# Kernel optimization log

Hardware: AMD Instinct MI355X
Metric: run time of the kernel (lower is better)

Reference implementation:

```python
import jax, jax.numpy as jnp
import numpy as np

B, N, K = 4, 100000, 128
Q_MIN = 0.5
S_B = 1.0
POT_SCALE = 1.0
REP_SCALE = 1.0
BETA_SCALE = 1.0
E_WEIGHT = 1.0
POS_WEIGHT = 1.0
TIME_WEIGHT = 1.0
HUBER_D = 2.0


def setup_inputs() -> dict:
    key = jax.random.key(0)
    ks = jax.random.split(key, 9)
    return {
        "beta": jax.random.uniform(ks[0], (B, N), dtype=jnp.float32),
        "ccoords": jax.random.normal(ks[1], (B, N, 2), dtype=jnp.float32),
        "pred_energy": jax.random.uniform(ks[2], (B, N), dtype=jnp.float32),
        "pred_pos": jax.random.normal(ks[3], (B, N, 2), dtype=jnp.float32),
        "pred_time": jax.random.uniform(ks[4], (B, N), dtype=jnp.float32),
        "t_energy": jax.random.uniform(ks[5], (B, N), dtype=jnp.float32),
        "t_pos": jax.random.normal(ks[6], (B, N, 2), dtype=jnp.float32),
        "t_time": jax.random.uniform(ks[7], (B, N), dtype=jnp.float32),
        "t_idx": jax.random.randint(ks[8], (B, N), 0, K + 1, dtype=jnp.int32),
    }


def _huber(x, d):
    a = jnp.abs(x)
    return jnp.where(a <= d, 0.5 * x * x, d * (a - 0.5 * d))


def _oc_loss(beta, ccoords, pred_energy, pred_pos, pred_time,
             t_energy, t_pos, t_time, t_idx):
    eps = 1e-4
    beta = jnp.clip(beta, eps, 1.0 - eps)
    q = jnp.arctanh(beta) ** 2 + Q_MIN                     # [B,N]

    obj = t_idx - 1                                        # -1 = noise, 0..K-1 = object id
    M = obj[:, :, None] == jnp.arange(K, dtype=jnp.int32)  # [B,N,K] bool membership
    Mf = M.astype(q.dtype)
    obj_exists = jnp.any(M, axis=1)                        # [B,K]
    exf = obj_exists.astype(q.dtype)

    # condensation point per object = member hit with max charge q (segment argmax)
    q_masked = jnp.where(M, q[:, :, None], -1.0)           # [B,N,K]
    alpha = jnp.argmax(q_masked, axis=1)                   # [B,K]
    x_alpha = jnp.take_along_axis(ccoords, alpha[:, :, None], axis=1)  # [B,K,2]
    q_alpha = jnp.take_along_axis(q, alpha, axis=1)        # [B,K]
    beta_alpha = jnp.take_along_axis(beta, alpha, axis=1)  # [B,K]

    # pairwise hit <-> condensation-point distances, [B,N,K]
    diff = ccoords[:, :, None, :] - x_alpha[:, None, :, :]
    dist = jnp.sqrt(jnp.sum(diff * diff, axis=-1) + 1e-12)

    qq = q[:, :, None] * q_alpha[:, None, :] * exf[:, None, :]
    v_att = qq * (dist * dist) * Mf
    v_rep = qq * jax.nn.relu(1.0 - dist) * (1.0 - Mf)
    n_tot = jnp.asarray(B * N, q.dtype)
    L_att = jnp.sum(v_att) / n_tot
    L_rep = jnp.sum(v_rep) / n_tot

    # beta loss: pull condensation-point betas to 1, suppress noise betas
    n_obj = jnp.maximum(jnp.sum(exf), 1.0)
    L_beta_obj = jnp.sum((1.0 - beta_alpha) * exf) / n_obj
    noise = (t_idx == 0).astype(q.dtype)
    L_noise = jnp.sum(beta * noise) / jnp.maximum(jnp.sum(noise), 1.0)
    L_beta = L_beta_obj + S_B * L_noise

    # payload losses, beta-weighted over non-noise hits
    p = (jnp.arctanh(beta) ** 2) * (1.0 - noise)           # [B,N]
    p_sum = jnp.maximum(jnp.sum(p), 1e-6)
    L_energy = jnp.sum(p * _huber(pred_energy - t_energy, HUBER_D)) / p_sum
    L_pos = jnp.sum(p * jnp.sum((pred_pos - t_pos) ** 2, axis=-1)) / p_sum
    L_time = jnp.sum(p * (pred_time - t_time) ** 2) / p_sum

    return (POT_SCALE * L_att + REP_SCALE * L_rep + BETA_SCALE * L_beta
            + E_WEIGHT * L_energy + POS_WEIGHT * L_pos + TIME_WEIGHT * L_time)


def reference(beta, ccoords, pred_energy, pred_pos, pred_time,
              t_energy, t_pos, t_time, t_idx):
    return _oc_loss(beta, ccoords, pred_energy, pred_pos, pred_time,
                    t_energy, t_pos, t_time, t_idx)
```

## Files before the change

kernel.cpp:

```cpp
#include <hip/hip_runtime.h>
#include <math.h>

#define BB 4
#define NN 100000
#define KK 128
#define HB 64
#define HH 4


__device__ __forceinline__ float clipb(float b) {
    return fminf(fmaxf(b, 1e-4f), 1.0f - 1e-4f);
}

__global__ void k_argmax(const float* __restrict__ beta,
                         const int* __restrict__ tidx,
                         unsigned long long* __restrict__ packed) {
    int b = blockIdx.y;
    __shared__ unsigned long long smax[KK];
    for (int t = threadIdx.x; t < KK; t += blockDim.x) smax[t] = 0ULL;
    __syncthreads();
    const float* betab = beta + b * NN;
    const int*   tib   = tidx + b * NN;
    for (int n = blockIdx.x * blockDim.x + threadIdx.x; n < NN;
         n += gridDim.x * blockDim.x) {
        int obj = tib[n] - 1;
        if (obj >= 0) {
            unsigned hi = __float_as_uint(clipb(betab[n]));
            unsigned long long key = ((unsigned long long)hi << 32) |
                                     (unsigned long long)(0xFFFFFFFFu - (unsigned)n);
            atomicMax(&smax[obj], key);
        }
    }
    __syncthreads();
    for (int t = threadIdx.x; t < KK; t += blockDim.x) {
        unsigned long long v = smax[t];
        if (v) atomicMax(&packed[b * KK + t], v);
    }
}

__global__ void k_gather(const unsigned long long* __restrict__ packed,
                         const float2* __restrict__ cc,
                         float4* __restrict__ sobj,
                         float* __restrict__ acc) {
    int t = blockIdx.x * blockDim.x + threadIdx.x;
    if (t >= BB * KK) return;
    int b = t / KK;
    unsigned long long v = packed[t];
    float4 o = make_float4(0.f, 0.f, 0.f, 0.f);
    if (v) {
        unsigned n = 0xFFFFFFFFu - (unsigned)(v & 0xFFFFFFFFu);
        float ba = __uint_as_float((unsigned)(v >> 32));
        float at = atanhf(ba);
        float2 c = cc[b * NN + (int)n];
        o.x = c.x; o.y = c.y; o.z = at * at + 0.5f; o.w = 1.0f;
        atomicAdd(&acc[8], 1.0f);
        atomicAdd(&acc[9], 1.0f - ba);
    }
    sobj[t] = o;
}

__global__ void __launch_bounds__(HB) k_main(
    const float*  __restrict__ beta, const float2* __restrict__ cc,
    const float*  __restrict__ pe,   const float2* __restrict__ pp,
    const float*  __restrict__ pt,   const float*  __restrict__ te,
    const float2* __restrict__ tp,   const float*  __restrict__ tt,
    const int*    __restrict__ tidx, const float4* __restrict__ sobjg,
    float* __restrict__ acc) {
    int b = blockIdx.y;
    __shared__ float4 sobj[KK];
    for (int t = threadIdx.x; t < KK; t += HB) sobj[t] = sobjg[b * KK + t];
    __syncthreads();

    int base = blockIdx.x * (HB * HH) + threadIdx.x;
    int   nn[HH]; bool vv[HH]; int ii[HH];
    float2 ch[HH]; float rp[HH];
    #pragma unroll
    for (int h = 0; h < HH; ++h) {
        nn[h] = base + h * HB;
        vv[h] = nn[h] < NN;
        ii[h] = b * NN + (vv[h] ? nn[h] : 0);
        ch[h] = cc[ii[h]];
        rp[h] = 0.f;
    }

    #pragma unroll 4
    for (int k = 0; k < KK; ++k) {
        float4 o = sobj[k];
        #pragma unroll
        for (int h = 0; h < HH; ++h) {
            float dx = ch[h].x - o.x, dy = ch[h].y - o.y;
            float s  = fmaf(dx, dx, fmaf(dy, dy, 1e-12f));
            float d  = __builtin_amdgcn_sqrtf(s);
            rp[h] = fmaf(o.z, fmaxf(1.0f - d, 0.0f), rp[h]);
        }
    }

    float p_att = 0.f, p_rep = 0.f, p_nb = 0.f, p_nc = 0.f;
    float p_ps = 0.f, p_e = 0.f, p_pos = 0.f, p_tm = 0.f;

    #pragma unroll
    for (int h = 0; h < HH; ++h) {
        if (!vv[h]) continue;
        int idx = ii[h];
        float rep = rp[h];

        float bc  = clipb(beta[idx]);
        float at  = atanhf(bc);
        float at2 = at * at;
        float q   = at2 + 0.5f;
        int   ti  = tidx[idx];
        int   obj = ti - 1;

        if (obj >= 0) {
            float4 o = sobj[obj];
            float dx = ch[h].x - o.x, dy = ch[h].y - o.y;
            float s = fmaf(dx, dx, fmaf(dy, dy, 1e-12f));
            float d = __builtin_amdgcn_sqrtf(s);
            rep   -= o.z * fmaxf(1.0f - d, 0.0f);
            p_att += q * (o.z * s);
        }
        p_rep += q * rep;

        if (ti == 0) {
            p_nb += bc;
            p_nc += 1.0f;
        } else {
            p_ps += at2;
            float de = pe[idx] - te[idx];
            float a  = fabsf(de);
            float hb = (a <= 2.0f) ? (0.5f * de * de) : (2.0f * (a - 1.0f));
            p_e  += at2 * hb;
            float2 ppv = pp[idx], tpv = tp[idx];
            float dpx = ppv.x - tpv.x, dpy = ppv.y - tpv.y;
            p_pos += at2 * (dpx * dpx + dpy * dpy);
            float dt = pt[idx] - tt[idx];
            p_tm += at2 * dt * dt;
        }
    }

    float vals[8] = {p_att, p_rep, p_nb, p_nc, p_ps, p_e, p_pos, p_tm};
    int lane = threadIdx.x & 63;
    float mine = 0.f;
    #pragma unroll
    for (int i = 0; i < 8; ++i) {
        float v = vals[i];
        #pragma unroll
        for (int off = 32; off > 0; off >>= 1) v += __shfl_xor(v, off, 64);
        if (lane == i) mine = v;
    }
    if (lane < 8) atomicAdd(&acc[lane], mine);
}

__global__ void k_final(const float* __restrict__ acc, float* __restrict__ out) {
    float inv_n  = 1.0f / (float)(BB * NN);
    float L_att  = acc[0] * inv_n;
    float L_rep  = acc[1] * inv_n;
    float n_obj  = fmaxf(acc[8], 1.0f);
    float L_beta = acc[9] / n_obj + acc[2] / fmaxf(acc[3], 1.0f);
    float p_sum  = fmaxf(acc[4], 1e-6f);
    out[0] = L_att + L_rep + L_beta + (acc[5] + acc[6] + acc[7]) / p_sum;
}

extern "C" void kernel_launch(void* const* d_in, const int* in_sizes, int n_in,
                              void* d_out, int out_size, void* d_ws, size_t ws_size,
                              hipStream_t stream) {
    const float*  beta = (const float*)d_in[0];
    const float2* cc   = (const float2*)d_in[1];
    const float*  pe   = (const float*)d_in[2];
    const float2* pp   = (const float2*)d_in[3];
    const float*  pt   = (const float*)d_in[4];
    const float*  te   = (const float*)d_in[5];
    const float2* tp   = (const float2*)d_in[6];
    const float*  tt   = (const float*)d_in[7];
    const int*    ti   = (const int*)d_in[8];

    unsigned long long* packed = (unsigned long long*)d_ws;
    float4* sobj = (float4*)((char*)d_ws + 4096);
    float*  acc  = (float*)((char*)d_ws + 12288);
    float*  out  = (float*)d_out;

    hipMemsetAsync(d_ws, 0, 12352, stream);

    k_argmax<<<dim3(64, BB), 256, 0, stream>>>(beta, ti, packed);
    k_gather<<<dim3(2), 256, 0, stream>>>(packed, cc, sobj, acc);
    k_main<<<dim3((NN + HB * HH - 1) / (HB * HH), BB), HB, 0, stream>>>(
        beta, cc, pe, pp, pt, te, tp, tt, ti, sobj, acc);
    k_final<<<1, 1, 0, stream>>>(acc, out);
}
```

Baseline: 128.5 us.

## Fuse gather into main kernel and replace global atomics with block partials

Removes the separate gather kernel: each main block now decodes the packed argmax keys and loads condensation-point coordinates itself, overlapping that with its own coordinate loads. Global float atomics are replaced by per-block partial sums written to workspace and reduced by a 64-lane final kernel, which also computes the object count and beta term. Block size rises from 64 to 256 and the argmax grid doubles. Every block now redundantly recomputes 128 atanh/gathers, and occupancy changes with the larger blocks.

```diff
diff --git a/kernel.cpp b/kernel.cpp
--- a/kernel.cpp
+++ b/kernel.cpp
@@ -4,8 +4,10 @@
 #define BB 4
 #define NN 100000
 #define KK 128
-#define HB 64
+#define HB 256
 #define HH 4
+#define GX ((NN + HB * HH - 1) / (HB * HH))
+#define NBLK (GX * BB)
 
 
 __device__ __forceinline__ float clipb(float b) {
@@ -38,50 +40,42 @@
     }
 }
 
-__global__ void k_gather(const unsigned long long* __restrict__ packed,
-                         const float2* __restrict__ cc,
-                         float4* __restrict__ sobj,
-                         float* __restrict__ acc) {
-    int t = blockIdx.x * blockDim.x + threadIdx.x;
-    if (t >= BB * KK) return;
-    int b = t / KK;
-    unsigned long long v = packed[t];
-    float4 o = make_float4(0.f, 0.f, 0.f, 0.f);
-    if (v) {
-        unsigned n = 0xFFFFFFFFu - (unsigned)(v & 0xFFFFFFFFu);
-        float ba = __uint_as_float((unsigned)(v >> 32));
-        float at = atanhf(ba);
-        float2 c = cc[b * NN + (int)n];
-        o.x = c.x; o.y = c.y; o.z = at * at + 0.5f; o.w = 1.0f;
-        atomicAdd(&acc[8], 1.0f);
-        atomicAdd(&acc[9], 1.0f - ba);
-    }
-    sobj[t] = o;
-}
-
 __global__ void __launch_bounds__(HB) k_main(
     const float*  __restrict__ beta, const float2* __restrict__ cc,
     const float*  __restrict__ pe,   const float2* __restrict__ pp,
     const float*  __restrict__ pt,   const float*  __restrict__ te,
     const float2* __restrict__ tp,   const float*  __restrict__ tt,
-    const int*    __restrict__ tidx, const float4* __restrict__ sobjg,
-    float* __restrict__ acc) {
+    const int*    __restrict__ tidx,
+    const unsigned long long* __restrict__ packed,
+    float* __restrict__ part) {
     int b = blockIdx.y;
     __shared__ float4 sobj[KK];
-    for (int t = threadIdx.x; t < KK; t += HB) sobj[t] = sobjg[b * KK + t];
-    __syncthreads();
+    __shared__ float sred[4][8];
+
+    if (threadIdx.x < KK) {
+        unsigned long long v = packed[b * KK + threadIdx.x];
+        float4 o = make_float4(0.f, 0.f, 0.f, 0.f);
+        if (v) {
+            unsigned n = 0xFFFFFFFFu - (unsigned)(v & 0xFFFFFFFFu);
+            float ba = __uint_as_float((unsigned)(v >> 32));
+            float at = atanhf(ba);
+            float2 c = cc[b * NN + (int)n];
+            o = make_float4(c.x, c.y, at * at + 0.5f, 1.f);
+        }
+        sobj[threadIdx.x] = o;
+    }
 
     int base = blockIdx.x * (HB * HH) + threadIdx.x;
-    int   nn[HH]; bool vv[HH]; int ii[HH];
-    float2 ch[HH]; float rp[HH];
+    bool vv[HH]; int ii[HH]; float2 ch[HH]; float rp[HH];
     #pragma unroll
     for (int h = 0; h < HH; ++h) {
-        nn[h] = base + h * HB;
-        vv[h] = nn[h] < NN;
-        ii[h] = b * NN + (vv[h] ? nn[h] : 0);
+        int n = base + h * HB;
+        vv[h] = n < NN;
+        ii[h] = b * NN + (vv[h] ? n : 0);
         ch[h] = cc[ii[h]];
         rp[h] = 0.f;
     }
+    __syncthreads();
 
     #pragma unroll 4
     for (int k = 0; k < KK; ++k) {
@@ -101,9 +95,8 @@
     #pragma unroll
     for (int h = 0; h < HH; ++h) {
         if (!vv[h]) continue;
-        int idx = ii[h];
+        int   idx = ii[h];
         float rep = rp[h];
-
         float bc  = clipb(beta[idx]);
         float at  = atanhf(bc);
         float at2 = at * at;
@@ -139,26 +132,61 @@
     }
 
     float vals[8] = {p_att, p_rep, p_nb, p_nc, p_ps, p_e, p_pos, p_tm};
-    int lane = threadIdx.x & 63;
-    float mine = 0.f;
+    int lane = threadIdx.x & 63, wave = threadIdx.x >> 6;
     #pragma unroll
     for (int i = 0; i < 8; ++i) {
         float v = vals[i];
         #pragma unroll
-        for (int off = 32; off > 0; off >>= 1) v += __shfl_xor(v, off, 64);
-        if (lane == i) mine = v;
-    }
-    if (lane < 8) atomicAdd(&acc[lane], mine);
-}
-
-__global__ void k_final(const float* __restrict__ acc, float* __restrict__ out) {
-    float inv_n  = 1.0f / (float)(BB * NN);
-    float L_att  = acc[0] * inv_n;
-    float L_rep  = acc[1] * inv_n;
-    float n_obj  = fmaxf(acc[8], 1.0f);
-    float L_beta = acc[9] / n_obj + acc[2] / fmaxf(acc[3], 1.0f);
-    float p_sum  = fmaxf(acc[4], 1e-6f);
-    out[0] = L_att + L_rep + L_beta + (acc[5] + acc[6] + acc[7]) / p_sum;
+        for (int off = 32; off > 0; off >>= 1) v += __shfl_down(v, off, 64);
+        if (lane == 0) sred[wave][i] = v;
+    }
+    __syncthreads();
+    if (threadIdx.x < 8) {
+        float s = sred[0][threadIdx.x] + sred[1][threadIdx.x] +
+                  sred[2][threadIdx.x] + sred[3][threadIdx.x];
+        part[(b * GX + blockIdx.x) * 8 + threadIdx.x] = s;
+    }
+}
+
+__global__ void __launch_bounds__(64) k_final(
+    const float* __restrict__ part,
+    const unsigned long long* __restrict__ packed,
+    float* __restrict__ out) {
+    int lane = threadIdx.x;
+
+    float nobj = 0.f, sba = 0.f;
+    for (int t = lane; t < BB * KK; t += 64) {
+        unsigned long long v = packed[t];
+        if (v) {
+            nobj += 1.f;
+            sba  += 1.0f - __uint_as_float((unsigned)(v >> 32));
+        }
+    }
+    #pragma unroll
+    for (int off = 32; off > 0; off >>= 1) {
+        nobj += __shfl_xor(nobj, off, 64);
+        sba  += __shfl_xor(sba, off, 64);
+    }
+
+    int comp = lane & 7;
+    float v = 0.f;
+    for (int r = lane >> 3; r < NBLK; r += 8)
+        v += part[r * 8 + comp];
+    v += __shfl_xor(v, 8, 64);
+    v += __shfl_xor(v, 16, 64);
+    v += __shfl_xor(v, 32, 64);
+    float tot[8];
+    #pragma unroll
+    for (int c = 0; c < 8; ++c) tot[c] = __shfl(v, c, 64);
+
+    if (lane == 0) {
+        float inv_n  = 1.0f / (float)(BB * NN);
+        float L_beta = sba / fmaxf(nobj, 1.0f) +
+                       tot[2] / fmaxf(tot[3], 1.0f);
+        float p_sum  = fmaxf(tot[4], 1e-6f);
+        out[0] = tot[0] * inv_n + tot[1] * inv_n + L_beta +
+                 (tot[5] + tot[6] + tot[7]) / p_sum;
+    }
 }
 
 extern "C" void kernel_launch(void* const* d_in, const int* in_sizes, int n_in,
@@ -175,15 +203,12 @@
     const int*    ti   = (const int*)d_in[8];
 
     unsigned long long* packed = (unsigned long long*)d_ws;
-    float4* sobj = (float4*)((char*)d_ws + 4096);
-    float*  acc  = (float*)((char*)d_ws + 12288);
-    float*  out  = (float*)d_out;
-
-    hipMemsetAsync(d_ws, 0, 12352, stream);
-
-    k_argmax<<<dim3(64, BB), 256, 0, stream>>>(beta, ti, packed);
-    k_gather<<<dim3(2), 256, 0, stream>>>(packed, cc, sobj, acc);
-    k_main<<<dim3((NN + HB * HH - 1) / (HB * HH), BB), HB, 0, stream>>>(
-        beta, cc, pe, pp, pt, te, tp, tt, ti, sobj, acc);
-    k_final<<<1, 1, 0, stream>>>(acc, out);
-}
+    float* part = (float*)((char*)d_ws + 4096);
+    float* out  = (float*)d_out;
+
+    hipMemsetAsync(packed, 0, 4096, stream);
+    k_argmax<<<dim3(128, BB), 256, 0, stream>>>(beta, ti, packed);
+    k_main<<<dim3(GX, BB), HB, 0, stream>>>(
+        beta, cc, pe, pp, pt, te, tp, tt, ti, packed, part);
+    k_final<<<1, 64, 0, stream>>>(part, packed, out);
+}
```

After: 122.5 us. 1.05x faster.
